# Kernel tuning notes

Hardware: AMD Instinct MI355X
Metric: run time of the kernel (lower is better)

## Reference

```python
import jax, jax.numpy as jnp
import numpy as np

C = 64
C8 = C // 8
N, H, W = 4, 512, 512


def conv1x1(x, w, b):
    # x: [N,C,H,W], w: [O,C], b: [O]
    return jnp.einsum('nchw,oc->nohw', x, w) + b[None, :, None, None]


def time_attention(x, qw, qb, kw, kb, vw, vb, gamma):
    # attention over the H axis; feature dim is (C//8)*W
    q = conv1x1(x, qw, qb)                     # [N,C8,H,W]
    k = conv1x1(x, kw, kb)                     # [N,C8,H,W]
    v = conv1x1(x, vw, vb)                     # [N,C,H,W]
    energy = jnp.einsum('nchw,ncgw->nhg', q, k)   # [N,H,H]
    attn = jax.nn.softmax(energy, axis=-1)
    out = jnp.einsum('ncgw,nhg->nchw', v, attn)   # [N,C,H,W]
    return gamma * out + x


def freq_attention(x, qw, qb, kw, kb, vw, vb, gamma):
    # attention over the W axis; feature dim is (C//8)*H
    q = conv1x1(x, qw, qb)
    k = conv1x1(x, kw, kb)
    v = conv1x1(x, vw, vb)
    energy = jnp.einsum('nchw,nchv->nwv', q, k)   # [N,W,W]
    attn = jax.nn.softmax(energy, axis=-1)
    out = jnp.einsum('nchv,nwv->nchw', v, attn)
    return gamma * out + x


def setup_inputs() -> dict:
    key = jax.random.key(0)
    ks = jax.random.split(key, 8)
    s = 0.05
    return {
        'x': jax.random.normal(ks[0], (N, C, H, W), dtype=jnp.float32),
        'tq_w': jax.random.normal(ks[1], (C8, C), dtype=jnp.float32) * s,
        'tq_b': jnp.zeros((C8,), jnp.float32),
        'tk_w': jax.random.normal(ks[2], (C8, C), dtype=jnp.float32) * s,
        'tk_b': jnp.zeros((C8,), jnp.float32),
        'tv_w': jax.random.normal(ks[3], (C, C), dtype=jnp.float32) * s,
        'tv_b': jnp.zeros((C,), jnp.float32),
        't_gamma': jnp.ones((1,), jnp.float32) * 0.5,
        'fq_w': jax.random.normal(ks[4], (C8, C), dtype=jnp.float32) * s,
        'fq_b': jnp.zeros((C8,), jnp.float32),
        'fk_w': jax.random.normal(ks[5], (C8, C), dtype=jnp.float32) * s,
        'fk_b': jnp.zeros((C8,), jnp.float32),
        'fv_w': jax.random.normal(ks[6], (C, C), dtype=jnp.float32) * s,
        'fv_b': jnp.zeros((C,), jnp.float32),
        'f_gamma': jnp.ones((1,), jnp.float32) * 0.5,
    }


def reference(x, tq_w, tq_b, tk_w, tk_b, tv_w, tv_b, t_gamma,
              fq_w, fq_b, fk_w, fk_b, fv_w, fv_b, f_gamma):
    t = time_attention(x, tq_w, tq_b, tk_w, tk_b, tv_w, tv_b, t_gamma)
    f = freq_attention(x, fq_w, fq_b, fk_w, fk_b, fv_w, fv_b, f_gamma)
    return x + t + f
```

## Files before the change

### kernel.cpp

```cpp
#include <hip/hip_runtime.h>
#include <stdint.h>

#define HW 262144
#define LDIM 512

typedef __bf16 bf16x8 __attribute__((ext_vector_type(8)));
typedef float f32x4 __attribute__((ext_vector_type(4)));
typedef short s16x8 __attribute__((ext_vector_type(8)));
typedef short s16x4 __attribute__((ext_vector_type(4)));

__device__ __forceinline__ unsigned short f2bf(float f) {
  union { float f; unsigned u; } v; v.f = f;
  unsigned r = v.u + 0x7fffu + ((v.u >> 16) & 1u);
  return (unsigned short)(r >> 16);
}

__device__ __forceinline__ float bf2f(short s) {
  union { unsigned u; float f; } v;
  v.u = ((unsigned)(unsigned short)s) << 16;
  return v.f;
}

__device__ __forceinline__ s16x8 pack_bf8(float4 a, float4 b) {
  s16x8 r;
  r[0] = (short)f2bf(a.x); r[1] = (short)f2bf(a.y);
  r[2] = (short)f2bf(a.z); r[3] = (short)f2bf(a.w);
  r[4] = (short)f2bf(b.x); r[5] = (short)f2bf(b.y);
  r[6] = (short)f2bf(b.z); r[7] = (short)f2bf(b.w);
  return r;
}

__device__ __forceinline__ f32x4 mfma16(bf16x8 a, bf16x8 b, f32x4 c) {
  return __builtin_amdgcn_mfma_f32_16x16x32_bf16(a, b, c, 0, 0, 0);
}

__device__ __forceinline__ void gl_lds16(const short* g, short* l) {
  __builtin_amdgcn_global_load_lds(
      (const __attribute__((address_space(1))) void*)g,
      (__attribute__((address_space(3))) void*)l, 16, 0, 0);
}

__global__ __launch_bounds__(256, 2) void conv_all_k(
    const float* __restrict__ x,
    const float* __restrict__ tqw, const float* __restrict__ tqb,
    const float* __restrict__ tkw, const float* __restrict__ tkb,
    const float* __restrict__ fqw, const float* __restrict__ fqb,
    const float* __restrict__ fkw, const float* __restrict__ fkb,
    const float* __restrict__ tvw, const float* __restrict__ fvw,
    short* __restrict__ QT, short* __restrict__ KT,
    short* __restrict__ QF, short* __restrict__ KF,
    short* __restrict__ Vt, short* __restrict__ Vf) {
  __shared__ __align__(16) short As[128 * 72];
  __shared__ __align__(16) short Ws[160 * 72];
  __shared__ float bia[32];
  int tid = threadIdx.x;
  int n = blockIdx.x >> 11;
  int p0 = (blockIdx.x & 2047) << 7;
#pragma unroll
  for (int i = 0; i < 5; ++i) {
    int idx = i * 256 + tid;
    int co = idx >> 3, k0 = (idx & 7) * 8;
    const float* wrow = (co < 8)  ? tqw + co * 64
                      : (co < 16) ? tkw + (co - 8) * 64
                      : (co < 24) ? fqw + (co - 16) * 64
                      : (co < 32) ? fkw + (co - 24) * 64
                      : (co < 96) ? tvw + (co - 32) * 64
                                  : fvw + (co - 96) * 64;
    float4 f0 = *(const float4*)(wrow + k0);
    float4 f1 = *(const float4*)(wrow + k0 + 4);
    *(s16x8*)(Ws + co * 72 + k0) = pack_bf8(f0, f1);
  }
  if (tid < 32) {
    const float* bsrc = (tid < 8) ? tqb : (tid < 16) ? tkb : (tid < 24) ? fqb : fkb;
    bia[tid] = bsrc[tid & 7];
  }
  {
    int mp = (tid & 31) * 4, k0 = (tid >> 5) * 8;
    const float* sp = x + ((size_t)(n * 64 + k0)) * HW + p0 + mp;
    s16x8 t0, t1, t2, t3;
#pragma unroll
    for (int j = 0; j < 8; ++j) {
      float4 v = *(const float4*)(sp + (size_t)j * HW);
      t0[j] = (short)f2bf(v.x); t1[j] = (short)f2bf(v.y);
      t2[j] = (short)f2bf(v.z); t3[j] = (short)f2bf(v.w);
    }
    *(s16x8*)(As + (mp + 0) * 72 + k0) = t0;
    *(s16x8*)(As + (mp + 1) * 72 + k0) = t1;
    *(s16x8*)(As + (mp + 2) * 72 + k0) = t2;
    *(s16x8*)(As + (mp + 3) * 72 + k0) = t3;
  }
  __syncthreads();
  int lane = tid & 63, wv = tid >> 6, fr = lane & 15, q = lane >> 4;
  int wm = wv * 32;
  f32x4 acc[2][10];
#pragma unroll
  for (int mi = 0; mi < 2; ++mi)
#pragma unroll
    for (int ni = 0; ni < 10; ++ni) acc[mi][ni] = (f32x4){0.f, 0.f, 0.f, 0.f};
#pragma unroll
  for (int ks = 0; ks < 2; ++ks) {
    bf16x8 af[2];
#pragma unroll
    for (int mi = 0; mi < 2; ++mi)
      af[mi] = *(const bf16x8*)(As + (wm + mi * 16 + fr) * 72 + ks * 32 + q * 8);
#pragma unroll
    for (int ni = 0; ni < 10; ++ni) {
      bf16x8 bw = *(const bf16x8*)(Ws + (ni * 16 + fr) * 72 + ks * 32 + q * 8);
      acc[0][ni] = mfma16(af[0], bw, acc[0][ni]);
      acc[1][ni] = mfma16(af[1], bw, acc[1][ni]);
    }
  }
#pragma unroll
  for (int mi = 0; mi < 2; ++mi)
#pragma unroll
    for (int ni = 0; ni < 10; ++ni) {
      int pl = wm + mi * 16 + q * 4;
      int co = ni * 16 + fr;
      float b = (co < 32) ? bia[co] : 0.f;
      short* dst;
      if (co < 32) {
        short* dd = (co < 8) ? QT : (co < 16) ? KT : (co < 24) ? QF : KF;
        dst = dd + ((size_t)(n * 8 + (co & 7))) * HW;
      } else if (co < 96) {
        dst = Vt + ((size_t)(n * 64 + (co - 32))) * HW;
      } else {
        dst = Vf + ((size_t)(n * 64 + (co - 96))) * HW;
      }
      s16x4 sv;
#pragma unroll
      for (int r = 0; r < 4; ++r) sv[r] = (short)f2bf(acc[mi][ni][r] + b);
      *(s16x4*)(dst + p0 + pl) = sv;
    }
}

__global__ __launch_bounds__(256, 4) void trans_k(short* __restrict__ V) {
  __shared__ short La[64][72];
  __shared__ short Lb[64][72];
  short* p = V + (size_t)blockIdx.y * HW;
  int b = blockIdx.x;
  int ti = 0;
  while (b >= 8 - ti) { b -= 8 - ti; ++ti; }
  int tj = ti + b;
  int tid = threadIdx.x;
  int hl = tid >> 4, wl = (tid & 15) * 4;
#pragma unroll
  for (int it = 0; it < 4; ++it) {
    int r = hl + it * 16;
    s16x4 va = *(const s16x4*)(p + (size_t)(ti * 64 + r) * 512 + tj * 64 + wl);
    La[wl + 0][r] = va[0]; La[wl + 1][r] = va[1];
    La[wl + 2][r] = va[2]; La[wl + 3][r] = va[3];
    if (ti != tj) {
      s16x4 vb = *(const s16x4*)(p + (size_t)(tj * 64 + r) * 512 + ti * 64 + wl);
      Lb[wl + 0][r] = vb[0]; Lb[wl + 1][r] = vb[1];
      Lb[wl + 2][r] = vb[2]; Lb[wl + 3][r] = vb[3];
    }
  }
  __syncthreads();
#pragma unroll
  for (int it = 0; it < 4; ++it) {
    int c = hl + it * 16;
    *(s16x4*)(p + (size_t)(tj * 64 + c) * 512 + ti * 64 + wl) =
        *(const s16x4*)(&La[c][wl]);
    if (ti != tj)
      *(s16x4*)(p + (size_t)(ti * 64 + c) * 512 + tj * 64 + wl) =
          *(const s16x4*)(&Lb[c][wl]);
  }
}

template<bool OBF>
__global__ __launch_bounds__(256, 4) void gemm_a(
    const short* __restrict__ A0, long az, int zshA,
    const short* __restrict__ B0, long bz, int zshB,
    void* __restrict__ C0, long cz) {
  __shared__ __align__(16) short As[128 * 32];
  __shared__ __align__(16) short Bs[128 * 32];
  int tid = threadIdx.x;
  int z = blockIdx.z;
  int m0g = blockIdx.y * 128, n0g = blockIdx.x * 128;
  const short* Abz = A0 + (size_t)(z >> zshA) * (size_t)az;
  const short* Bbz = B0 + (size_t)(z >> zshB) * (size_t)bz;
  int lane = tid & 63, wv = tid >> 6;
  int wm = (wv >> 1) * 64, wn = (wv & 1) * 64;
  int fr = lane & 15, q = lane >> 4;

  int srow = lane >> 2;
  int sch = (lane & 3) * 8;
  const short* ga0 = Abz + (size_t)(m0g + wv * 32 + srow) * 512 + sch;
  const short* ga1 = ga0 + 16 * 512;
  const short* gb0 = Bbz + (size_t)(n0g + wv * 32 + srow) * 512 + sch;
  const short* gb1 = gb0 + 16 * 512;
  short* la0 = As + (wv * 32) * 32;
  short* la1 = As + (wv * 32 + 16) * 32;
  short* lb0 = Bs + (wv * 32) * 32;
  short* lb1 = Bs + (wv * 32 + 16) * 32;

  f32x4 acc[4][4];
#pragma unroll
  for (int mi = 0; mi < 4; ++mi)
#pragma unroll
    for (int ni = 0; ni < 4; ++ni) acc[mi][ni] = (f32x4){0.f, 0.f, 0.f, 0.f};

  for (int kk = 0; kk < 512; kk += 32) {
    gl_lds16(ga0 + kk, la0);
    gl_lds16(ga1 + kk, la1);
    gl_lds16(gb0 + kk, lb0);
    gl_lds16(gb1 + kk, lb1);
    __syncthreads();
    bf16x8 af[4], bg[4];
#pragma unroll
    for (int mi = 0; mi < 4; ++mi)
      af[mi] = *(const bf16x8*)(As + (wm + mi * 16 + fr) * 32 + q * 8);
#pragma unroll
    for (int ni = 0; ni < 4; ++ni)
      bg[ni] = *(const bf16x8*)(Bs + (wn + ni * 16 + fr) * 32 + q * 8);
#pragma unroll
    for (int mi = 0; mi < 4; ++mi)
#pragma unroll
      for (int ni = 0; ni < 4; ++ni)
        acc[mi][ni] = mfma16(af[mi], bg[ni], acc[mi][ni]);
    __syncthreads();
  }

  size_t coff = (size_t)z * (size_t)cz;
#pragma unroll
  for (int mi = 0; mi < 4; ++mi)
#pragma unroll
    for (int ni = 0; ni < 4; ++ni) {
      int row = m0g + wm + mi * 16 + q * 4;
      int col = n0g + wn + ni * 16 + fr;
#pragma unroll
      for (int r = 0; r < 4; ++r) {
        float v = acc[mi][ni][r];
        if constexpr (OBF) {
          ((short*)C0)[coff + (size_t)(row + r) * LDIM + col] = (short)f2bf(v);
        } else {
          ((float*)C0)[coff + (size_t)(row + r) * LDIM + col] = v;
        }
      }
    }
}

__global__ __launch_bounds__(256, 2) void gemm_t(
    const short* __restrict__ A0, long az,
    const short* __restrict__ B0, long bz,
    float* __restrict__ C0, long cz) {
  __shared__ __align__(16) short As[128 * 40];
  __shared__ __align__(16) short Bs[128 * 40];
  int tid = threadIdx.x;
  int z = blockIdx.z;
  int m0g = blockIdx.y * 128, n0g = blockIdx.x * 128;
  const short* Abz = A0 + (size_t)z * (size_t)az;
  const short* Bbz = B0 + (size_t)z * (size_t)bz;
  int lane = tid & 63, wv = tid >> 6;
  int wm = (wv >> 1) * 64, wn = (wv & 1) * 64;
  int fr = lane & 15, q = lane >> 4;
  int mp = (tid & 63) * 2, k0 = (tid >> 6) * 8;

  f32x4 acc[4][4];
#pragma unroll
  for (int mi = 0; mi < 4; ++mi)
#pragma unroll
    for (int ni = 0; ni < 4; ++ni) acc[mi][ni] = (f32x4){0.f, 0.f, 0.f, 0.f};

  for (int kk = 0; kk < 512; kk += 32) {
    {
      const short* s = Abz + (size_t)(kk + k0) * 512 + m0g + mp;
      s16x8 c0, c1;
#pragma unroll
      for (int j = 0; j < 8; ++j) {
        unsigned v = *(const unsigned*)(s + (size_t)j * 512);
        c0[j] = (short)(v & 0xffffu);
        c1[j] = (short)(v >> 16);
      }
      *(s16x8*)(As + mp * 40 + k0) = c0;
      *(s16x8*)(As + (mp + 1) * 40 + k0) = c1;
    }
    {
      const short* s = Bbz + (size_t)(kk + k0) * 512 + n0g + mp;
      s16x8 c0, c1;
#pragma unroll
      for (int j = 0; j < 8; ++j) {
        unsigned v = *(const unsigned*)(s + (size_t)j * 512);
        c0[j] = (short)(v & 0xffffu);
        c1[j] = (short)(v >> 16);
      }
      *(s16x8*)(Bs + mp * 40 + k0) = c0;
      *(s16x8*)(Bs + (mp + 1) * 40 + k0) = c1;
    }
    __syncthreads();
    bf16x8 af[4], bg[4];
#pragma unroll
    for (int mi = 0; mi < 4; ++mi)
      af[mi] = *(const bf16x8*)(As + (wm + mi * 16 + fr) * 40 + q * 8);
#pragma unroll
    for (int ni = 0; ni < 4; ++ni)
      bg[ni] = *(const bf16x8*)(Bs + (wn + ni * 16 + fr) * 40 + q * 8);
#pragma unroll
    for (int mi = 0; mi < 4; ++mi)
#pragma unroll
      for (int ni = 0; ni < 4; ++ni)
        acc[mi][ni] = mfma16(af[mi], bg[ni], acc[mi][ni]);
    __syncthreads();
  }

  size_t coff = (size_t)z * (size_t)cz;
#pragma unroll
  for (int mi = 0; mi < 4; ++mi)
#pragma unroll
    for (int ni = 0; ni < 4; ++ni) {
      int row = m0g + wm + mi * 16 + q * 4;
      int col = n0g + wn + ni * 16 + fr;
#pragma unroll
      for (int r = 0; r < 4; ++r)
        C0[coff + (size_t)(row + r) * LDIM + col] = acc[mi][ni][r];
    }
}

__global__ __launch_bounds__(256, 4) void softmax8_k(const float* __restrict__ Ep,
                                                     const float* __restrict__ gp,
                                                     short* __restrict__ A) {
  int tid = threadIdx.x;
  int lane = tid & 63, wv = tid >> 6;
  int row = blockIdx.x * 4 + wv;
  int n = row >> 9, h = row & 511;
  const float* base = Ep + (size_t)(n * 8) * HW + (size_t)h * 512 + lane * 8;
  float v[8] = {0.f, 0.f, 0.f, 0.f, 0.f, 0.f, 0.f, 0.f};
#pragma unroll
  for (int cc = 0; cc < 8; ++cc) {
    const float* e = base + (size_t)cc * HW;
    float4 a = *(const float4*)e;
    float4 b = *(const float4*)(e + 4);
    v[0] += a.x; v[1] += a.y; v[2] += a.z; v[3] += a.w;
    v[4] += b.x; v[5] += b.y; v[6] += b.z; v[7] += b.w;
  }
  float m = v[0];
#pragma unroll
  for (int j = 1; j < 8; ++j) m = fmaxf(m, v[j]);
#pragma unroll
  for (int off = 32; off >= 1; off >>= 1) m = fmaxf(m, __shfl_xor(m, off));
  float s = 0.f;
#pragma unroll
  for (int j = 0; j < 8; ++j) {
    v[j] = __expf(v[j] - m);
    s += v[j];
  }
#pragma unroll
  for (int off = 32; off >= 1; off >>= 1) s += __shfl_xor(s, off);
  float sc = gp[0] / s;
  s16x8 o;
#pragma unroll
  for (int j = 0; j < 8; ++j) o[j] = (short)f2bf(v[j] * sc);
  *(s16x8*)(A + (size_t)row * LDIM + lane * 8) = o;
}

__global__ __launch_bounds__(256, 4) void gemm_tf(
    const short* __restrict__ At, const short* __restrict__ VtT,
    const short* __restrict__ Vf, const short* __restrict__ Af,
    const float* __restrict__ x,
    const float* __restrict__ tvb, const float* __restrict__ fvb,
    const float* __restrict__ tg, const float* __restrict__ fg,
    float* __restrict__ out, int Z) {
  __shared__ __align__(16) short As[128 * 32];
  __shared__ __align__(16) short Bs[128 * 32];
  int tid = threadIdx.x;
  int f = blockIdx.x;
  int xcd = f & 7, j = f >> 3;
  int yt = j & 3;
  int pid = xcd * (Z >> 1) + (j >> 2);
  int nt = pid & 3, z = pid >> 2;
  int n = z >> 6, o = z & 63;
  int m0g = yt * 128, n0g = nt * 128;

  int lane = tid & 63, wv = tid >> 6;
  int wm = (wv >> 1) * 64, wn = (wv & 1) * 64;
  int fr = lane & 15, q = lane >> 4;
  int srow = lane >> 2;
  int sch = (lane & 3) * 8;
  short* la0 = As + (wv * 32) * 32;
  short* la1 = la0 + 16 * 32;
  short* lb0 = Bs + (wv * 32) * 32;
  short* lb1 = lb0 + 16 * 32;

  f32x4 acc[4][4];
#pragma unroll
  for (int mi = 0; mi < 4; ++mi)
#pragma unroll
    for (int ni = 0; ni < 4; ++ni) acc[mi][ni] = (f32x4){0.f, 0.f, 0.f, 0.f};

  const short* g1a = At + (size_t)n * HW + (size_t)(m0g + wv * 32 + srow) * 512 + sch;
  const short* g1b = VtT + (size_t)z * HW + (size_t)(n0g + wv * 32 + srow) * 512 + sch;
  for (int kk = 0; kk < 512; kk += 32) {
    gl_lds16(g1a + kk, la0);
    gl_lds16(g1a + kk + 16 * 512, la1);
    gl_lds16(g1b + kk, lb0);
    gl_lds16(g1b + kk + 16 * 512, lb1);
    __syncthreads();
    bf16x8 af[4], bg[4];
#pragma unroll
    for (int mi = 0; mi < 4; ++mi)
      af[mi] = *(const bf16x8*)(As + (wm + mi * 16 + fr) * 32 + q * 8);
#pragma unroll
    for (int ni = 0; ni < 4; ++ni)
      bg[ni] = *(const bf16x8*)(Bs + (wn + ni * 16 + fr) * 32 + q * 8);
#pragma unroll
    for (int mi = 0; mi < 4; ++mi)
#pragma unroll
      for (int ni = 0; ni < 4; ++ni)
        acc[mi][ni] = mfma16(af[mi], bg[ni], acc[mi][ni]);
    __syncthreads();
  }
  const short* g2a = Vf + (size_t)z * HW + (size_t)(m0g + wv * 32 + srow) * 512 + sch;
  const short* g2b = Af + (size_t)n * HW + (size_t)(n0g + wv * 32 + srow) * 512 + sch;
  for (int kk = 0; kk < 512; kk += 32) {
    gl_lds16(g2a + kk, la0);
    gl_lds16(g2a + kk + 16 * 512, la1);
    gl_lds16(g2b + kk, lb0);
    gl_lds16(g2b + kk + 16 * 512, lb1);
    __syncthreads();
    bf16x8 af[4], bg[4];
#pragma unroll
    for (int mi = 0; mi < 4; ++mi)
      af[mi] = *(const bf16x8*)(As + (wm + mi * 16 + fr) * 32 + q * 8);
#pragma unroll
    for (int ni = 0; ni < 4; ++ni)
      bg[ni] = *(const bf16x8*)(Bs + (wn + ni * 16 + fr) * 32 + q * 8);
#pragma unroll
    for (int mi = 0; mi < 4; ++mi)
#pragma unroll
      for (int ni = 0; ni < 4; ++ni)
        acc[mi][ni] = mfma16(af[mi], bg[ni], acc[mi][ni]);
    __syncthreads();
  }

  float cb = tg[0] * tvb[o] + fg[0] * fvb[o];
  size_t zoff = (size_t)z * HW;
#pragma unroll
  for (int mi = 0; mi < 4; ++mi)
#pragma unroll
    for (int ni = 0; ni < 4; ++ni) {
      int row = m0g + wm + mi * 16 + q * 4;
      int col = n0g + wn + ni * 16 + fr;
#pragma unroll
      for (int r = 0; r < 4; ++r) {
        size_t idx = zoff + (size_t)(row + r) * LDIM + col;
        out[idx] = 3.f * x[idx] + acc[mi][ni][r] + cb;
      }
    }
}

extern "C" void kernel_launch(void* const* d_in, const int* in_sizes, int n_in,
                              void* d_out, int out_size, void* d_ws, size_t ws_size,
                              hipStream_t stream) {
  (void)in_sizes; (void)n_in; (void)out_size;
  const float* x   = (const float*)d_in[0];
  const float* tqw = (const float*)d_in[1];
  const float* tqb = (const float*)d_in[2];
  const float* tkw = (const float*)d_in[3];
  const float* tkb = (const float*)d_in[4];
  const float* tvw = (const float*)d_in[5];
  const float* tvb = (const float*)d_in[6];
  const float* tg  = (const float*)d_in[7];
  const float* fqw = (const float*)d_in[8];
  const float* fqb = (const float*)d_in[9];
  const float* fkw = (const float*)d_in[10];
  const float* fkb = (const float*)d_in[11];
  const float* fvw = (const float*)d_in[12];
  const float* fvb = (const float*)d_in[13];
  const float* fg  = (const float*)d_in[14];
  float* out = (float*)d_out;

  const size_t per_n = ((size_t)64 * HW * 2) * 2
                     + ((size_t)8 * HW * 2) * 4;
  int nb = (ws_size >= 4 * per_n) ? 4
         : (ws_size >= 2 * per_n) ? 2 : 1;

  char* wb = (char*)d_ws;
  size_t sz_v  = (size_t)nb * 64 * HW * 2;
  size_t sz_qk = (size_t)nb * 8 * HW * 2;
  short* Vt = (short*)(wb);
  short* Vf = (short*)(wb + sz_v);
  short* QT = (short*)(wb + 2 * sz_v);
  short* KT = (short*)(wb + 2 * sz_v + sz_qk);
  short* QF = (short*)(wb + 2 * sz_v + 2 * sz_qk);
  short* KF = (short*)(wb + 2 * sz_v + 3 * sz_qk);
  short* At = QT;
  short* Af = QF;

  for (int n0 = 0; n0 < 4; n0 += nb) {
    const float* xn = x + (size_t)n0 * 64 * HW;
    float* outn = out + (size_t)n0 * 64 * HW;
    float* EbT = outn;
    float* EbF = outn + (size_t)nb * 8 * HW;

    conv_all_k<<<dim3(nb * 2048), dim3(256), 0, stream>>>(
        xn, tqw, tqb, tkw, tkb, fqw, fqb, fkw, fkb, tvw, fvw,
        QT, KT, QF, KF, Vt, Vf);
    trans_k<<<dim3(36, nb * 64), dim3(256), 0, stream>>>(Vt);
    gemm_a<false><<<dim3(4, 4, nb * 8), dim3(256), 0, stream>>>(
        QT, (long)HW, 0, KT, (long)HW, 0, EbT, (long)HW);
    softmax8_k<<<dim3(nb * 128), dim3(256), 0, stream>>>(EbT, tg, At);
    gemm_t<<<dim3(4, 4, nb * 8), dim3(256), 0, stream>>>(
        QF, (long)HW, KF, (long)HW, EbF, (long)HW);
    softmax8_k<<<dim3(nb * 128), dim3(256), 0, stream>>>(EbF, fg, Af);
    gemm_tf<<<dim3(16 * nb * 64), dim3(256), 0, stream>>>(
        At, Vt, Vf, Af, xn, tvb, fvb, tg, fg, outn, nb * 64);
  }
}
```

Measured before the change: 952.5 us.

## Double-buffer LDS tiles in GEMM kernels and swizzle LDS layout in gemm_tf

Both GEMM kernels now keep two LDS buffers and issue the global-to-LDS loads for the next k-slice before computing on the current one. This replaces the two barriers per iteration with a single one, so global load latency can overlap the MFMA work. gemm_tf also merges its two K loops into one 32-step pipelined loop and applies an XOR swizzle to the LDS column chunk on both write and read, aiming to reduce bank conflicts. LDS use per block doubles, which may lower occupancy under the 4-blocks launch bound.

Measured after the change: 868.0 us. 1.1x faster.

```diff
diff --git a/kernel.cpp b/kernel.cpp
--- a/kernel.cpp
+++ b/kernel.cpp
@@ -172,8 +172,8 @@
     const short* __restrict__ A0, long az, int zshA,
     const short* __restrict__ B0, long bz, int zshB,
     void* __restrict__ C0, long cz) {
-  __shared__ __align__(16) short As[128 * 32];
-  __shared__ __align__(16) short Bs[128 * 32];
+  __shared__ __align__(16) short As[2][128 * 32];
+  __shared__ __align__(16) short Bs[2][128 * 32];
   int tid = threadIdx.x;
   int z = blockIdx.z;
   int m0g = blockIdx.y * 128, n0g = blockIdx.x * 128;
@@ -186,13 +186,8 @@
   int srow = lane >> 2;
   int sch = (lane & 3) * 8;
   const short* ga0 = Abz + (size_t)(m0g + wv * 32 + srow) * 512 + sch;
-  const short* ga1 = ga0 + 16 * 512;
   const short* gb0 = Bbz + (size_t)(n0g + wv * 32 + srow) * 512 + sch;
-  const short* gb1 = gb0 + 16 * 512;
-  short* la0 = As + (wv * 32) * 32;
-  short* la1 = As + (wv * 32 + 16) * 32;
-  short* lb0 = Bs + (wv * 32) * 32;
-  short* lb1 = Bs + (wv * 32 + 16) * 32;
+  int lofs = (wv * 32) * 32;
 
   f32x4 acc[4][4];
 #pragma unroll
@@ -200,19 +195,30 @@
 #pragma unroll
     for (int ni = 0; ni < 4; ++ni) acc[mi][ni] = (f32x4){0.f, 0.f, 0.f, 0.f};
 
-  for (int kk = 0; kk < 512; kk += 32) {
-    gl_lds16(ga0 + kk, la0);
-    gl_lds16(ga1 + kk, la1);
-    gl_lds16(gb0 + kk, lb0);
-    gl_lds16(gb1 + kk, lb1);
-    __syncthreads();
+  gl_lds16(ga0, As[0] + lofs);
+  gl_lds16(ga0 + 16 * 512, As[0] + lofs + 16 * 32);
+  gl_lds16(gb0, Bs[0] + lofs);
+  gl_lds16(gb0 + 16 * 512, Bs[0] + lofs + 16 * 32);
+  __syncthreads();
+
+#pragma unroll 2
+  for (int s = 0; s < 16; ++s) {
+    int p = s & 1;
+    if (s < 15) {
+      const short* ga = ga0 + (s + 1) * 32;
+      const short* gb = gb0 + (s + 1) * 32;
+      gl_lds16(ga, As[p ^ 1] + lofs);
+      gl_lds16(ga + 16 * 512, As[p ^ 1] + lofs + 16 * 32);
+      gl_lds16(gb, Bs[p ^ 1] + lofs);
+      gl_lds16(gb + 16 * 512, Bs[p ^ 1] + lofs + 16 * 32);
+    }
     bf16x8 af[4], bg[4];
 #pragma unroll
     for (int mi = 0; mi < 4; ++mi)
-      af[mi] = *(const bf16x8*)(As + (wm + mi * 16 + fr) * 32 + q * 8);
+      af[mi] = *(const bf16x8*)(As[p] + (wm + mi * 16 + fr) * 32 + q * 8);
 #pragma unroll
     for (int ni = 0; ni < 4; ++ni)
-      bg[ni] = *(const bf16x8*)(Bs + (wn + ni * 16 + fr) * 32 + q * 8);
+      bg[ni] = *(const bf16x8*)(Bs[p] + (wn + ni * 16 + fr) * 32 + q * 8);
 #pragma unroll
     for (int mi = 0; mi < 4; ++mi)
 #pragma unroll
@@ -360,8 +366,8 @@
     const float* __restrict__ tvb, const float* __restrict__ fvb,
     const float* __restrict__ tg, const float* __restrict__ fg,
     float* __restrict__ out, int Z) {
-  __shared__ __align__(16) short As[128 * 32];
-  __shared__ __align__(16) short Bs[128 * 32];
+  __shared__ __align__(16) short As[2][128 * 32];
+  __shared__ __align__(16) short Bs[2][128 * 32];
   int tid = threadIdx.x;
   int f = blockIdx.x;
   int xcd = f & 7, j = f >> 3;
@@ -375,55 +381,46 @@
   int wm = (wv >> 1) * 64, wn = (wv & 1) * 64;
   int fr = lane & 15, q = lane >> 4;
   int srow = lane >> 2;
-  int sch = (lane & 3) * 8;
-  short* la0 = As + (wv * 32) * 32;
-  short* la1 = la0 + 16 * 32;
-  short* lb0 = Bs + (wv * 32) * 32;
-  short* lb1 = lb0 + 16 * 32;
-
-  f32x4 acc[4][4];
-#pragma unroll
-  for (int mi = 0; mi < 4; ++mi)
-#pragma unroll
-    for (int ni = 0; ni < 4; ++ni) acc[mi][ni] = (f32x4){0.f, 0.f, 0.f, 0.f};
+  int sch = ((lane & 3) ^ ((lane >> 3) & 3)) * 8;
+  int lofs = (wv * 32) * 32;
+  int sq = (q ^ ((fr >> 1) & 3)) * 8;
 
   const short* g1a = At + (size_t)n * HW + (size_t)(m0g + wv * 32 + srow) * 512 + sch;
   const short* g1b = VtT + (size_t)z * HW + (size_t)(n0g + wv * 32 + srow) * 512 + sch;
-  for (int kk = 0; kk < 512; kk += 32) {
-    gl_lds16(g1a + kk, la0);
-    gl_lds16(g1a + kk + 16 * 512, la1);
-    gl_lds16(g1b + kk, lb0);
-    gl_lds16(g1b + kk + 16 * 512, lb1);
-    __syncthreads();
-    bf16x8 af[4], bg[4];
-#pragma unroll
-    for (int mi = 0; mi < 4; ++mi)
-      af[mi] = *(const bf16x8*)(As + (wm + mi * 16 + fr) * 32 + q * 8);
-#pragma unroll
-    for (int ni = 0; ni < 4; ++ni)
-      bg[ni] = *(const bf16x8*)(Bs + (wn + ni * 16 + fr) * 32 + q * 8);
-#pragma unroll
-    for (int mi = 0; mi < 4; ++mi)
-#pragma unroll
-      for (int ni = 0; ni < 4; ++ni)
-        acc[mi][ni] = mfma16(af[mi], bg[ni], acc[mi][ni]);
-    __syncthreads();
-  }
   const short* g2a = Vf + (size_t)z * HW + (size_t)(m0g + wv * 32 + srow) * 512 + sch;
   const short* g2b = Af + (size_t)n * HW + (size_t)(n0g + wv * 32 + srow) * 512 + sch;
-  for (int kk = 0; kk < 512; kk += 32) {
-    gl_lds16(g2a + kk, la0);
-    gl_lds16(g2a + kk + 16 * 512, la1);
-    gl_lds16(g2b + kk, lb0);
-    gl_lds16(g2b + kk + 16 * 512, lb1);
-    __syncthreads();
+
+  f32x4 acc[4][4];
+#pragma unroll
+  for (int mi = 0; mi < 4; ++mi)
+#pragma unroll
+    for (int ni = 0; ni < 4; ++ni) acc[mi][ni] = (f32x4){0.f, 0.f, 0.f, 0.f};
+
+  gl_lds16(g1a, As[0] + lofs);
+  gl_lds16(g1a + 16 * 512, As[0] + lofs + 16 * 32);
+  gl_lds16(g1b, Bs[0] + lofs);
+  gl_lds16(g1b + 16 * 512, Bs[0] + lofs + 16 * 32);
+  __syncthreads();
+
+#pragma unroll 2
+  for (int s = 0; s < 32; ++s) {
+    int p = s & 1;
+    if (s < 31) {
+      int t = s + 1;
+      const short* ga = (t < 16) ? g1a + t * 32 : g2a + (t - 16) * 32;
+      const short* gb = (t < 16) ? g1b + t * 32 : g2b + (t - 16) * 32;
+      gl_lds16(ga, As[p ^ 1] + lofs);
+      gl_lds16(ga + 16 * 512, As[p ^ 1] + lofs + 16 * 32);
+      gl_lds16(gb, Bs[p ^ 1] + lofs);
+      gl_lds16(gb + 16 * 512, Bs[p ^ 1] + lofs + 16 * 32);
+    }
     bf16x8 af[4], bg[4];
 #pragma unroll
     for (int mi = 0; mi < 4; ++mi)
-      af[mi] = *(const bf16x8*)(As + (wm + mi * 16 + fr) * 32 + q * 8);
+      af[mi] = *(const bf16x8*)(As[p] + (wm + mi * 16 + fr) * 32 + sq);
 #pragma unroll
     for (int ni = 0; ni < 4; ++ni)
-      bg[ni] = *(const bf16x8*)(Bs + (wn + ni * 16 + fr) * 32 + q * 8);
+      bg[ni] = *(const bf16x8*)(Bs[p] + (wn + ni * 16 + fr) * 32 + sq);
 #pragma unroll
     for (int mi = 0; mi < 4; ++mi)
 #pragma unroll
```
